# Performance work log

Measured on AMD Instinct MI355X. Metric: run time of the kernel, lower is better.

Reference implementation:

```python
import jax, jax.numpy as jnp
import numpy as np


def conv(x, w, b=None, pad=0):
    y = jax.lax.conv_general_dilated(x, w, (1, 1), [(pad, pad), (pad, pad)],
                                     dimension_numbers=('NCHW', 'OIHW', 'NCHW'))
    if b is not None:
        y = y + b[None, :, None, None]
    return y


def bn(x, g, b, m, v, eps=1e-5):
    scale = g / jnp.sqrt(v + eps)
    return (x - m[None, :, None, None]) * scale[None, :, None, None] + b[None, :, None, None]


def channel_gate(x, w1, b1, w2, b2):
    # avg pool -> MLP -> sigmoid, returns [B, C, 1, 1]
    p = x.mean(axis=(2, 3))                       # [B, C]
    h = jax.nn.relu(p @ w1.T + b1)                # [B, C//r]
    a = h @ w2.T + b2                             # [B, C]
    return jax.nn.sigmoid(a)[:, :, None, None]


def setup_inputs() -> dict:
    key = jax.random.key(0)
    ks = iter(jax.random.split(key, 48))
    B, Cin, H, W = 2, 256, 64, 64
    Ci = Cin // 2          # inter_channels = 128
    Cr = Ci // 16          # gate bottleneck = 8
    def nrm(shape, s=0.05):
        return jax.random.normal(next(ks), shape, jnp.float32) * s
    d = {}
    d['q'] = jax.random.normal(next(ks), (B, Cin, H, W), jnp.float32)
    d['s'] = jax.random.normal(next(ks), (B, Cin, H, W), jnp.float32)
    # Trans_s: conv3x3 + BN
    d['ts_w'] = nrm((Ci, Cin, 3, 3)); d['ts_b'] = jnp.zeros(Ci)
    d['ts_g'] = jnp.ones(Ci); d['ts_be'] = jnp.zeros(Ci)
    d['ts_m'] = nrm((Ci,), 0.01); d['ts_v'] = jnp.ones(Ci)
    # Trans_q: conv3x3 + BN
    d['tq_w'] = nrm((Ci, Cin, 3, 3)); d['tq_b'] = jnp.zeros(Ci)
    d['tq_g'] = jnp.ones(Ci); d['tq_be'] = jnp.zeros(Ci)
    d['tq_m'] = nrm((Ci,), 0.01); d['tq_v'] = jnp.ones(Ci)
    # common_v 1x1
    d['cv_w'] = nrm((Ci, Ci, 1, 1)); d['cv_b'] = jnp.zeros(Ci)
    # key/query 1x1 projections (out = Ci//2)
    d['k1_w'] = nrm((Ci // 2, Ci, 1, 1)); d['k1_b'] = jnp.zeros(Ci // 2)
    d['q1_w'] = nrm((Ci // 2, Ci, 1, 1)); d['q1_b'] = jnp.zeros(Ci // 2)
    d['k2_w'] = nrm((Ci // 2, Ci, 1, 1)); d['k2_b'] = jnp.zeros(Ci // 2)
    d['q2_w'] = nrm((Ci // 2, Ci, 1, 1)); d['q2_b'] = jnp.zeros(Ci // 2)
    # ChannelGate MLP
    d['g1_w'] = nrm((Cr, Ci)); d['g1_b'] = jnp.zeros(Cr)
    d['g2_w'] = nrm((Ci, Cr)); d['g2_b'] = jnp.zeros(Ci)
    # conv_cat: conv3x3 (no bias) + BN
    d['cc_w'] = nrm((Ci, 2 * Ci, 3, 3))
    d['cc_g'] = jnp.ones(Ci); d['cc_be'] = jnp.zeros(Ci)
    d['cc_m'] = nrm((Ci,), 0.01); d['cc_v'] = jnp.ones(Ci)
    return d


def reference(q, s, ts_w, ts_b, ts_g, ts_be, ts_m, ts_v,
              tq_w, tq_b, tq_g, tq_be, tq_m, tq_v,
              cv_w, cv_b, k1_w, k1_b, q1_w, q1_b, k2_w, k2_b, q2_w, q2_b,
              g1_w, g1_b, g2_w, g2_b, cc_w, cc_g, cc_be, cc_m, cc_v):
    # stems: conv3x3 + BN + ReLU
    s = jax.nn.relu(bn(conv(s, ts_w, ts_b, pad=1), ts_g, ts_be, ts_m, ts_v))
    q = jax.nn.relu(bn(conv(q, tq_w, tq_b, pad=1), tq_g, tq_be, tq_m, tq_v))
    B, C, H, W = q.shape
    N = H * W
    # values
    v_q1 = conv(q, cv_w, cv_b)                          # [B,C,H,W]
    v_s1 = conv(s, cv_w, cv_b)
    v_q = v_q1.reshape(B, C, N).transpose(0, 2, 1)      # [B,N,C]
    v_s = v_s1.reshape(B, C, N).transpose(0, 2, 1)
    # dual keys / queries with negation trick
    k1 = conv(s, k1_w, k1_b).reshape(B, C // 2, N)
    k2 = conv(q, k2_w, k2_b).reshape(B, C // 2, N)
    key_cat = jnp.concatenate([k1, -k2], axis=1).transpose(0, 2, 1)   # [B,N,C]
    q1x = conv(s, q1_w, q1_b).reshape(B, C // 2, N)
    q2x = conv(q, q2_w, q2_b).reshape(B, C // 2, N)
    query_cat = jnp.concatenate([q1x, q2x], axis=1)                    # [B,C,N]
    # abs-score attention, dual softmax from the same score matrix
    A_s = jnp.abs(jnp.einsum('bnc,bcm->bnm', key_cat, query_cat))      # [B,N,N]
    att_s = jax.nn.softmax(A_s, axis=-1)
    att_q = jax.nn.softmax(A_s.transpose(0, 2, 1), axis=-1)
    # attend + channel-gate SE fusion + residual
    p_s = jnp.einsum('bnm,bmc->bnc', att_s, v_s).transpose(0, 2, 1).reshape(B, C, H, W)
    E_s = channel_gate(v_s1, g1_w, g1_b, g2_w, g2_b) * p_s + s
    q_s = jnp.einsum('bnm,bmc->bnc', att_q, v_q).transpose(0, 2, 1).reshape(B, C, H, W)
    E_q = channel_gate(v_q1, g1_w, g1_b, g2_w, g2_b) * q_s + q
    # concat + conv3x3(no bias) + BN + ReLU
    cpam = jax.nn.relu(bn(conv(jnp.concatenate([E_q, E_s], axis=1), cc_w, None, pad=1),
                          cc_g, cc_be, cc_m, cc_v))
    return (cpam, E_q, E_s)
```

## Files before the change

### kernel.cpp

```cpp
#include <hip/hip_runtime.h>

typedef __bf16 bf16;
typedef __bf16 v8bf __attribute__((ext_vector_type(8)));
typedef __bf16 v4bf __attribute__((ext_vector_type(4)));
typedef float v4f __attribute__((ext_vector_type(4)));

#define MFMA16(a, b, c) __builtin_amdgcn_mfma_f32_16x16x32_bf16(a, b, c, 0, 0, 0)

__device__ __forceinline__ float sf(float x) {
  if (!(x == x)) return 0.f;
  return fminf(fmaxf(x, -1e30f), 1e30f);
}

__global__ __launch_bounds__(256) void fill_kernel(float* __restrict__ out, float v, int n) {
  int i = blockIdx.x * 256 + threadIdx.x;
  if (i < n) out[i] = v;
}

__global__ __launch_bounds__(256) void prep_kernel(
    const float* __restrict__ ts_w, const float* __restrict__ tq_w,
    const float* ts_b, const float* ts_g, const float* ts_be, const float* ts_m, const float* ts_v,
    const float* tq_b, const float* tq_g, const float* tq_be, const float* tq_m, const float* tq_v,
    bf16* __restrict__ Wt01, float* __restrict__ ss01)
{
  int idx = blockIdx.x * 256 + threadIdx.x;
  if (idx < 589824) {
    int which = idx / 294912;
    int rem = idx - which * 294912;
    int co = rem / 2304;
    int r2 = rem - co * 2304;
    int tap = r2 >> 8;
    int ci = r2 & 255;
    const float* W = which ? tq_w : ts_w;
    Wt01[idx] = (bf16)W[(co * 256 + ci) * 9 + tap];
  } else if (idx < 590080) {
    int i = idx - 589824;
    int which = i >> 7, c = i & 127;
    float g, be, m, vv, bias;
    if (which == 0) { g=ts_g[c]; be=ts_be[c]; m=ts_m[c]; vv=ts_v[c]; bias=ts_b[c]; }
    else            { g=tq_g[c]; be=tq_be[c]; m=tq_m[c]; vv=tq_v[c]; bias=tq_b[c]; }
    float scale = g / sqrtf(vv + 1e-5f);
    ss01[which * 256 + c] = sf(scale);
    ss01[which * 256 + 128 + c] = sf((bias - m) * scale + be);
  }
}

__global__ __launch_bounds__(256) void prep2_kernel(
    const float* __restrict__ cc_w, const float* cc_g, const float* cc_be,
    const float* cc_m, const float* cc_v,
    bf16* __restrict__ Wt2, float* __restrict__ ss_cc)
{
  int idx = blockIdx.x * 256 + threadIdx.x;
  if (idx < 294912) {
    int co = idx / 2304;
    int r2 = idx - co * 2304;
    int tap = r2 >> 8;
    int ci = r2 & 255;
    Wt2[idx] = (bf16)cc_w[(co * 256 + ci) * 9 + tap];
  } else if (idx < 295040) {
    int c = idx - 294912;
    float scale = cc_g[c] / sqrtf(cc_v[c] + 1e-5f);
    ss_cc[c] = sf(scale);
    ss_cc[128 + c] = sf(-cc_m[c] * scale + cc_be[c]);
  }
}

__global__ __launch_bounds__(256) void convN_kernel(
    const float* __restrict__ pS, const float* __restrict__ pQ,
    const bf16* __restrict__ Wb, const float* __restrict__ ssb,
    void* __restrict__ out_, int mode)
{
  __shared__ bf16 As[66][40];
  __shared__ bf16 Bs[3][64][40];

  int y = blockIdx.x;
  int co0 = blockIdx.y * 64;
  int z = blockIdx.z;
  int tsr = z >> 1, b = z & 1;

  const float *in0, *in1;
  const bf16* W;
  const float* sp;
  if (mode == 0) {
    const float* base = (tsr ? pQ : pS) + (long)b * 1048576;
    in0 = base; in1 = base + 524288;
    W = Wb + (long)tsr * 294912;
    sp = ssb + tsr * 256;
  } else {
    in0 = pS + 1048576 + (long)b * 524288;
    in1 = pS + 2097152 + (long)b * 524288;
    W = Wb; sp = ssb;
  }

  int t = threadIdx.x, lane = t & 63, w = t >> 6;
  int l15 = lane & 15, l4 = lane >> 4;
  int wr = (w & 1) * 32, wc = (w >> 1) * 32;
  int ac = t & 31, ag = t >> 5;
  int bco = t >> 2, bk = (t & 3) * 8;

  v4f acc[2][2] = {};

  auto loadA = [&](int it, v8bf& areg) {
    int dy = it >> 3, ks = it & 7;
    int ysrc = y + dy - 1;
    int cg = ks * 32 + ac;
    const float* ip = (cg < 128) ? (in0 + (long)cg * 4096) : (in1 + (long)(cg - 128) * 4096);
    if ((unsigned)ysrc < 64u) {
      const float* src = ip + ysrc * 64 + ag * 8;
#pragma unroll
      for (int i = 0; i < 8; ++i) areg[i] = (bf16)src[i];
    } else {
#pragma unroll
      for (int i = 0; i < 8; ++i) areg[i] = (bf16)0.f;
    }
  };
  auto loadB = [&](int it, v8bf* breg) {
    int dy = it >> 3, ks = it & 7;
    const bf16* wk = W + (long)(co0 + bco) * 2304 + dy * 3 * 256 + ks * 32 + bk;
#pragma unroll
    for (int d = 0; d < 3; ++d) breg[d] = *(const v8bf*)(wk + d * 256);
  };

  v8bf areg, breg[3];
  loadA(0, areg);
  loadB(0, breg);

  for (int it = 0; it < 24; ++it) {
    __syncthreads();
#pragma unroll
    for (int i = 0; i < 8; ++i) As[ag * 8 + 1 + i][ac] = areg[i];
    if (ag == 0) As[0][ac] = (bf16)0.f;
    if (ag == 7) As[65][ac] = (bf16)0.f;
#pragma unroll
    for (int d = 0; d < 3; ++d) *(v8bf*)&Bs[d][bco][bk] = breg[d];
    __syncthreads();
    if (it < 23) { loadA(it + 1, areg); loadB(it + 1, breg); }
#pragma unroll
    for (int d = 0; d < 3; ++d) {
      v8bf af0 = *(const v8bf*)&As[wr + d + l15][l4 * 8];
      v8bf af1 = *(const v8bf*)&As[wr + 16 + d + l15][l4 * 8];
#pragma unroll
      for (int j = 0; j < 2; ++j) {
        v8bf bfr = *(const v8bf*)&Bs[d][wc + j * 16 + l15][l4 * 8];
        acc[0][j] = MFMA16(af0, bfr, acc[0][j]);
        acc[1][j] = MFMA16(af1, bfr, acc[1][j]);
      }
    }
  }
#pragma unroll
  for (int i = 0; i < 2; ++i) {
    int nb = y * 64 + wr + i * 16 + l4 * 4;
#pragma unroll
    for (int j = 0; j < 2; ++j) {
      int c = co0 + wc + j * 16 + l15;
      float scale = sp[c], shift = sp[128 + c];
      if (mode == 0) {
        bf16* o = (bf16*)out_ + ((long)(tsr * 2 + b) * 4096 + nb) * 128 + c;
#pragma unroll
        for (int r = 0; r < 4; ++r)
          o[r * 128] = (bf16)sf(fmaxf(acc[i][j][r] * scale + shift, 0.f));
      } else {
        v4f pk;
#pragma unroll
        for (int r = 0; r < 4; ++r)
          pk[r] = sf(fmaxf(acc[i][j][r] * scale + shift, 0.f));
        *(v4f*)((float*)out_ + ((long)b * 128 + c) * 4096 + nb) = pk;
      }
    }
  }
}

__global__ __launch_bounds__(256) void conv1_kernel(
    const bf16* __restrict__ feat_base,
    const float* __restrict__ cv_w, const float* __restrict__ k1_w, const float* __restrict__ q1_w,
    const float* __restrict__ k2_w, const float* __restrict__ q2_w,
    const float* __restrict__ cv_b, const float* __restrict__ k1_b, const float* __restrict__ q1_b,
    const float* __restrict__ k2_b, const float* __restrict__ q2_b,
    bf16* __restrict__ v_base, bf16* __restrict__ keyT, bf16* __restrict__ queryT,
    float* __restrict__ pmean)
{
  int nt = blockIdx.x;
  int br = blockIdx.z >> 1, b = blockIdx.z & 1;
  long zid = br * 2 + b;
  const bf16* feat = feat_base + zid * 524288 + (long)nt * 4096;

  __shared__ bf16 As[32][40];
  __shared__ bf16 Bs[256][40];

  int t = threadIdx.x, lane = t & 63, w = t >> 6;
  int l15 = lane & 15, l4 = lane >> 4;
  int wr = (w & 1) * 16, wc = (w >> 1) * 128;

  const float* wrow;
  bool negk = false;
  if (t < 128)       wrow = cv_w + (long)t * 128;
  else if (t < 192) { wrow = (br ? k2_w : k1_w) + (long)(t - 128) * 128; negk = (br != 0); }
  else               wrow = (br ? q2_w : q1_w) + (long)(t - 192) * 128;

  v4f acc[8] = {};
  int ap = t >> 2, ak = (t & 3) * 8;

  for (int ks = 0; ks < 4; ++ks) {
    int ci0 = ks * 32;
    v8bf av;
    if (t < 128) av = *(const v8bf*)(feat + ap * 128 + ci0 + ak);
    float wv[32];
#pragma unroll
    for (int u = 0; u < 32; ++u) wv[u] = wrow[ci0 + u];
    if (negk) {
#pragma unroll
      for (int u = 0; u < 32; ++u) wv[u] = -wv[u];
    }
    __syncthreads();
    if (t < 128) *(v8bf*)&As[ap][ak] = av;
#pragma unroll
    for (int u = 0; u < 32; ++u) Bs[t][u] = (bf16)wv[u];
    __syncthreads();
    v8bf af = *(const v8bf*)&As[wr + l15][l4 * 8];
#pragma unroll
    for (int j = 0; j < 8; ++j) {
      v8bf bfr = *(const v8bf*)&Bs[wc + j * 16 + l15][l4 * 8];
      acc[j] = MFMA16(af, bfr, acc[j]);
    }
  }

  int nb = nt * 32 + wr + l4 * 4;
#pragma unroll
  for (int j = 0; j < 8; ++j) {
    int c = wc + j * 16 + l15;
    float bv;
    if (c < 128)      bv = cv_b[c];
    else if (c < 192) bv = br ? -k2_b[c - 128] : k1_b[c - 128];
    else              bv = (br ? q2_b : q1_b)[c - 192];
    float v0 = sf(acc[j][0] + bv), v1 = sf(acc[j][1] + bv);
    float v2 = sf(acc[j][2] + bv), v3 = sf(acc[j][3] + bv);
    if (c < 128) {
      long off = (long)(nb >> 5) * 4096 + (c >> 4) * 512 + ((nb >> 3) & 3) * 128 +
                 (c & 15) * 8 + (nb & 7);
      v4bf pk;
      pk[0] = (bf16)v0; pk[1] = (bf16)v1; pk[2] = (bf16)v2; pk[3] = (bf16)v3;
      *(v4bf*)(v_base + zid * 524288 + off) = pk;
      float s = v0 + v1 + v2 + v3;
      s += __shfl_xor(s, 16, 64);
      s += __shfl_xor(s, 32, 64);
      if (l4 == 0) atomicAdd(&pmean[zid * 128 + c], s);
    } else if (c < 192) {
      int cc = (c - 128) + br * 64;
      long off = (long)(nb >> 4) * 2048 + (cc >> 5) * 512 + ((cc >> 3) & 3) * 128 +
                 (nb & 15) * 8 + (cc & 7);
      bf16* kp = keyT + (long)b * 524288 + off;
      kp[0] = (bf16)v0; kp[8] = (bf16)v1; kp[16] = (bf16)v2; kp[24] = (bf16)v3;
    } else {
      int cc = (c - 192) + br * 64;
      long off = (long)(nb >> 4) * 2048 + (cc >> 5) * 512 + ((cc >> 3) & 3) * 128 +
                 (nb & 15) * 8 + (cc & 7);
      bf16* qp = queryT + (long)b * 524288 + off;
      qp[0] = (bf16)v0; qp[8] = (bf16)v1; qp[16] = (bf16)v2; qp[24] = (bf16)v3;
    }
  }
}

__global__ __launch_bounds__(128) void gate2_kernel(
    const float* __restrict__ pmean, const float* __restrict__ g1_w, const float* __restrict__ g1_b,
    const float* __restrict__ g2_w, const float* __restrict__ g2_b, float* __restrict__ gate)
{
  __shared__ float p[128];
  __shared__ float h[8];
  int z = blockIdx.x, t = threadIdx.x;
  p[t] = pmean[z * 128 + t] * (1.f / 4096.f);
  __syncthreads();
  if (t < 8) {
    float a = g1_b[t];
    for (int c = 0; c < 128; ++c) a += g1_w[t * 128 + c] * p[c];
    h[t] = fmaxf(a, 0.f);
  }
  __syncthreads();
  float a = g2_b[t];
#pragma unroll
  for (int j = 0; j < 8; ++j) a += g2_w[t * 8 + j] * h[j];
  gate[z * 128 + t] = sf(1.f / (1.f + __expf(-a)));
}

__global__ __launch_bounds__(256, 2) void apply_kernel(
    const bf16* __restrict__ keyT, const bf16* __restrict__ queryT,
    const bf16* __restrict__ v_base, const float* __restrict__ gate,
    const bf16* __restrict__ feat_base, float* __restrict__ d_out)
{
  int nt = blockIdx.x, br = blockIdx.z >> 1, b = blockIdx.z & 1;
  int n0 = nt * 32;
  const bf16* Xf = (br ? queryT : keyT) + (long)b * 524288 + (long)(n0 >> 4) * 2048;
  const bf16* Yf = (br ? keyT : queryT) + (long)b * 524288;
  const bf16* Vf = v_base + (long)(br * 2 + b) * 524288;
  const float* gt = gate + (br * 2 + b) * 128;
  const bf16* feat = feat_base + (long)(br * 2 + b) * 524288 + (long)n0 * 128;

  __shared__ bf16 Ps[2][32][72];
  __shared__ float rps[4][32];

  int t = threadIdx.x, lane = t & 63, w = t >> 6;
  int l15 = lane & 15, l4 = lane >> 4;
  int wm = w * 16;
  int wr = (w & 1) * 16;
  int wc = (w >> 1) * 64;

  v8bf af[2][4];
#pragma unroll
  for (int i = 0; i < 2; ++i)
#pragma unroll
    for (int k = 0; k < 4; ++k)
      af[i][k] = *(const v8bf*)(Xf + i * 2048 + k * 512 + lane * 8);

  v4f acc[4] = {};
  float rp[2][4] = {};

  auto loadBy = [&](int m0, v8bf* by) {
    const bf16* p = Yf + (long)((m0 >> 4) + w) * 2048 + lane * 8;
#pragma unroll
    for (int k = 0; k < 4; ++k) by[k] = *(const v8bf*)(p + k * 512);
  };
  auto loadVb = [&](int m0, v8bf* vb) {
    const bf16* p = Vf + (long)(m0 >> 5) * 4096 + ((w >> 1) * 4) * 512 + lane * 8;
#pragma unroll
    for (int j = 0; j < 4; ++j)
#pragma unroll
      for (int k = 0; k < 2; ++k)
        vb[j * 2 + k] = *(const v8bf*)(p + k * 4096 + j * 512);
  };

  v8bf byA[4], byB[4], vbA[8], vbB[8];
  loadBy(0, byA);
  loadVb(0, vbA);

  auto subiter = [&](v8bf (&by)[4], v8bf (&vb)[8], v8bf (&byN)[4], v8bf (&vbN)[8],
                     int psb, int m0n, bool pf) {
    v4f sacc[2] = {};
#pragma unroll
    for (int k = 0; k < 4; ++k)
#pragma unroll
      for (int i = 0; i < 2; ++i)
        sacc[i] = MFMA16(af[i][k], by[k], sacc[i]);
    if (pf) { loadBy(m0n, byN); loadVb(m0n, vbN); }
#pragma unroll
    for (int i = 0; i < 2; ++i)
#pragma unroll
      for (int r = 0; r < 4; ++r) {
        float e = __expf(fminf(fabsf(sacc[i][r]), 80.f) - 50.f);
        rp[i][r] += e;
        Ps[psb][i * 16 + l4 * 4 + r][wm + l15] = (bf16)e;
      }
    asm volatile("s_waitcnt lgkmcnt(0)" ::: "memory");
    __builtin_amdgcn_s_barrier();
#pragma unroll
    for (int k = 0; k < 2; ++k) {
      v8bf p0 = *(const v8bf*)&Ps[psb][wr + l15][k * 32 + l4 * 8];
#pragma unroll
      for (int j = 0; j < 4; ++j)
        acc[j] = MFMA16(p0, vb[j * 2 + k], acc[j]);
    }
  };

  for (int mt2 = 0; mt2 < 32; ++mt2) {
    int mA = mt2 * 128;
    subiter(byA, vbA, byB, vbB, 0, mA + 64, true);
    subiter(byB, vbB, byA, vbA, 1, mA + 128, mt2 < 31);
  }

#pragma unroll
  for (int i = 0; i < 2; ++i)
#pragma unroll
    for (int r = 0; r < 4; ++r) {
      float v = rp[i][r];
      v += __shfl_xor(v, 1, 64);
      v += __shfl_xor(v, 2, 64);
      v += __shfl_xor(v, 4, 64);
      v += __shfl_xor(v, 8, 64);
      if (l15 == 0) rps[w][i * 16 + l4 * 4 + r] = v;
    }
  __syncthreads();

  float* outE = d_out + (long)(br ? 1 : 2) * 1048576 + (long)b * 524288;
  int rowt = wr + l4 * 4;
  float dv[4];
#pragma unroll
  for (int r = 0; r < 4; ++r)
    dv[r] = fmaxf(rps[0][rowt + r] + rps[1][rowt + r] + rps[2][rowt + r] + rps[3][rowt + r],
                  1e-30f);
#pragma unroll
  for (int j = 0; j < 4; ++j) {
    int c = wc + j * 16 + l15;
    float g = gt[c];
    v4f pk;
#pragma unroll
    for (int r = 0; r < 4; ++r) {
      float val = acc[j][r] / dv[r] * g + (float)feat[(long)(rowt + r) * 128 + c];
      pk[r] = sf(val);
    }
    *(v4f*)(outE + (long)c * 4096 + n0 + rowt) = pk;
  }
}

extern "C" void kernel_launch(void* const* d_in, const int* in_sizes, int n_in,
                              void* d_out, int out_size, void* d_ws, size_t ws_size,
                              hipStream_t stream)
{
  if (n_in != 33 || in_sizes[0] != 2097152 || in_sizes[2] != 294912 ||
      in_sizes[14] != 16384 || out_size != 3145728) {
    fill_kernel<<<12288, 256, 0, stream>>>((float*)d_out, 100.0f, 3145728);
    return;
  }
  if (ws_size < 12582912) {
    fill_kernel<<<12288, 256, 0, stream>>>((float*)d_out, 1.0f, 3145728);
    return;
  }

  const float* q_in = (const float*)d_in[0];
  const float* s_in = (const float*)d_in[1];
  char* ob = (char*)d_out;
  float* outf = (float*)d_out;

  float* gate  = (float*)(ob + 0);
  float* pmean = (float*)(ob + 2048);

  char* ws = (char*)d_ws;
  bf16*  sfeat  = (bf16*)(ws + 0);
  bf16*  vs     = (bf16*)(ws + 4194304);
  bf16*  keyT   = (bf16*)(ws + 8388608);
  bf16*  queryT = (bf16*)(ws + 10485760);
  bf16*  Wt01   = (bf16*)(ws + 8388608);
  float* ss01   = (float*)(ws + 10485760);
  bf16*  Wt2    = (bf16*)(ws + 0);
  float* ss_cc  = (float*)(ws + 589824);

  prep_kernel<<<2306, 256, 0, stream>>>(
      (const float*)d_in[2], (const float*)d_in[8],
      (const float*)d_in[3], (const float*)d_in[4], (const float*)d_in[5],
      (const float*)d_in[6], (const float*)d_in[7],
      (const float*)d_in[9], (const float*)d_in[10], (const float*)d_in[11],
      (const float*)d_in[12], (const float*)d_in[13],
      Wt01, ss01);

  fill_kernel<<<2, 256, 0, stream>>>(pmean, 0.0f, 512);

  convN_kernel<<<dim3(64, 2, 4), 256, 0, stream>>>(s_in, q_in, Wt01, ss01, sfeat, 0);

  conv1_kernel<<<dim3(128, 1, 4), 256, 0, stream>>>(
      sfeat,
      (const float*)d_in[14], (const float*)d_in[16], (const float*)d_in[18],
      (const float*)d_in[20], (const float*)d_in[22],
      (const float*)d_in[15], (const float*)d_in[17], (const float*)d_in[19],
      (const float*)d_in[21], (const float*)d_in[23],
      vs, keyT, queryT, pmean);

  gate2_kernel<<<4, 128, 0, stream>>>(pmean, (const float*)d_in[24], (const float*)d_in[25],
                                      (const float*)d_in[26], (const float*)d_in[27], gate);

  apply_kernel<<<dim3(128, 1, 4), 256, 0, stream>>>(keyT, queryT, vs, gate, sfeat, outf);

  prep2_kernel<<<1153, 256, 0, stream>>>(
      (const float*)d_in[28], (const float*)d_in[29], (const float*)d_in[30],
      (const float*)d_in[31], (const float*)d_in[32], Wt2, ss_cc);

  convN_kernel<<<dim3(64, 2, 2), 256, 0, stream>>>(outf, nullptr, Wt2, ss_cc, outf, 1);
}
```

Baseline: 275.3 us.

## Pre-transpose conv inputs to channel-last bf16 for vectorized A loads

Adds a transpose kernel that converts the s and q inputs from NCHW fp32 into a channel-last bf16 buffer placed in the output region. The 3x3 conv kernel then loads its A tile as single 16-byte vectors instead of eight strided fp32 loads with conversion, and writes shared memory with one vector store. The apply kernel now also writes its fused E outputs back into the bf16 feature buffer in channel-last layout, so the final conv reads bf16 from workspace rather than fp32 NCHW from the output. This costs an extra transpose pass and extra bf16 writes, and it relocates the Wt2 and ss_cc scratch buffers.

```diff
diff --git a/kernel.cpp b/kernel.cpp
--- a/kernel.cpp
+++ b/kernel.cpp
@@ -65,8 +65,27 @@
   }
 }
 
+__global__ __launch_bounds__(256) void tr_kernel(
+    const float* __restrict__ s_in, const float* __restrict__ q_in, bf16* __restrict__ xin)
+{
+  int nb = blockIdx.x;
+  int z = blockIdx.y;
+  const float* in = ((z >> 1) ? q_in : s_in) + (long)(z & 1) * 1048576;
+  bf16* out = xin + (long)z * 1048576;
+  int t = threadIdx.x, lane = t & 63, w = t >> 6;
+  long n = (long)nb * 64 + lane;
+#pragma unroll
+  for (int i = 0; i < 8; ++i) {
+    int c8 = w * 8 + i;
+    v8bf o;
+#pragma unroll
+    for (int j = 0; j < 8; ++j) o[j] = (bf16)in[(long)(c8 * 8 + j) * 4096 + n];
+    *(v8bf*)(out + n * 256 + c8 * 8) = o;
+  }
+}
+
 __global__ __launch_bounds__(256) void convN_kernel(
-    const float* __restrict__ pS, const float* __restrict__ pQ,
+    const bf16* __restrict__ inA,
     const bf16* __restrict__ Wb, const float* __restrict__ ssb,
     void* __restrict__ out_, int mode)
 {
@@ -78,24 +97,24 @@
   int z = blockIdx.z;
   int tsr = z >> 1, b = z & 1;
 
-  const float *in0, *in1;
+  const bf16 *in0, *in1;
   const bf16* W;
   const float* sp;
   if (mode == 0) {
-    const float* base = (tsr ? pQ : pS) + (long)b * 1048576;
-    in0 = base; in1 = base + 524288;
+    in0 = inA + (long)z * 1048576;
+    in1 = nullptr;
     W = Wb + (long)tsr * 294912;
     sp = ssb + tsr * 256;
   } else {
-    in0 = pS + 1048576 + (long)b * 524288;
-    in1 = pS + 2097152 + (long)b * 524288;
+    in0 = inA + (long)(2 + b) * 524288;
+    in1 = inA + (long)b * 524288;
     W = Wb; sp = ssb;
   }
 
   int t = threadIdx.x, lane = t & 63, w = t >> 6;
   int l15 = lane & 15, l4 = lane >> 4;
   int wr = (w & 1) * 32, wc = (w >> 1) * 32;
-  int ac = t & 31, ag = t >> 5;
+  int ax = t >> 2, ac0 = (t & 3) * 8;
   int bco = t >> 2, bk = (t & 3) * 8;
 
   v4f acc[2][2] = {};
@@ -103,12 +122,14 @@
   auto loadA = [&](int it, v8bf& areg) {
     int dy = it >> 3, ks = it & 7;
     int ysrc = y + dy - 1;
-    int cg = ks * 32 + ac;
-    const float* ip = (cg < 128) ? (in0 + (long)cg * 4096) : (in1 + (long)(cg - 128) * 4096);
     if ((unsigned)ysrc < 64u) {
-      const float* src = ip + ysrc * 64 + ag * 8;
-#pragma unroll
-      for (int i = 0; i < 8; ++i) areg[i] = (bf16)src[i];
+      long n = (long)ysrc * 64 + ax;
+      int cg = ks * 32 + ac0;
+      const bf16* src;
+      if (mode == 0)     src = in0 + n * 256 + cg;
+      else if (cg < 128) src = in0 + n * 128 + cg;
+      else               src = in1 + n * 128 + (cg - 128);
+      areg = *(const v8bf*)src;
     } else {
 #pragma unroll
       for (int i = 0; i < 8; ++i) areg[i] = (bf16)0.f;
@@ -121,16 +142,16 @@
     for (int d = 0; d < 3; ++d) breg[d] = *(const v8bf*)(wk + d * 256);
   };
 
+  if (t < 32) As[0][t] = (bf16)0.f;
+  else if (t < 64) As[65][t - 32] = (bf16)0.f;
+
   v8bf areg, breg[3];
   loadA(0, areg);
   loadB(0, breg);
 
   for (int it = 0; it < 24; ++it) {
     __syncthreads();
-#pragma unroll
-    for (int i = 0; i < 8; ++i) As[ag * 8 + 1 + i][ac] = areg[i];
-    if (ag == 0) As[0][ac] = (bf16)0.f;
-    if (ag == 7) As[65][ac] = (bf16)0.f;
+    *(v8bf*)&As[ax + 1][ac0] = areg;
 #pragma unroll
     for (int d = 0; d < 3; ++d) *(v8bf*)&Bs[d][bco][bk] = breg[d];
     __syncthreads();
@@ -284,7 +305,7 @@
 __global__ __launch_bounds__(256, 2) void apply_kernel(
     const bf16* __restrict__ keyT, const bf16* __restrict__ queryT,
     const bf16* __restrict__ v_base, const float* __restrict__ gate,
-    const bf16* __restrict__ feat_base, float* __restrict__ d_out)
+    bf16* __restrict__ feat_base, float* __restrict__ d_out)
 {
   int nt = blockIdx.x, br = blockIdx.z >> 1, b = blockIdx.z & 1;
   int n0 = nt * 32;
@@ -292,7 +313,7 @@
   const bf16* Yf = (br ? keyT : queryT) + (long)b * 524288;
   const bf16* Vf = v_base + (long)(br * 2 + b) * 524288;
   const float* gt = gate + (br * 2 + b) * 128;
-  const bf16* feat = feat_base + (long)(br * 2 + b) * 524288 + (long)n0 * 128;
+  bf16* feat = feat_base + (long)(br * 2 + b) * 524288 + (long)n0 * 128;
 
   __shared__ bf16 Ps[2][32][72];
   __shared__ float rps[4][32];
@@ -392,8 +413,11 @@
     v4f pk;
 #pragma unroll
     for (int r = 0; r < 4; ++r) {
-      float val = acc[j][r] / dv[r] * g + (float)feat[(long)(rowt + r) * 128 + c];
-      pk[r] = sf(val);
+      long fi = (long)(rowt + r) * 128 + c;
+      float fv = (float)feat[fi];
+      float val = sf(acc[j][r] / dv[r] * g + fv);
+      pk[r] = val;
+      feat[fi] = (bf16)val;
     }
     *(v4f*)(outE + (long)c * 4096 + n0 + rowt) = pk;
   }
@@ -420,6 +444,7 @@
 
   float* gate  = (float*)(ob + 0);
   float* pmean = (float*)(ob + 2048);
+  bf16*  xin   = (bf16*)(ob + 4194304);
 
   char* ws = (char*)d_ws;
   bf16*  sfeat  = (bf16*)(ws + 0);
@@ -428,8 +453,8 @@
   bf16*  queryT = (bf16*)(ws + 10485760);
   bf16*  Wt01   = (bf16*)(ws + 8388608);
   float* ss01   = (float*)(ws + 10485760);
-  bf16*  Wt2    = (bf16*)(ws + 0);
-  float* ss_cc  = (float*)(ws + 589824);
+  bf16*  Wt2    = (bf16*)(ws + 8388608);
+  float* ss_cc  = (float*)(ws + 8978432);
 
   prep_kernel<<<2306, 256, 0, stream>>>(
       (const float*)d_in[2], (const float*)d_in[8],
@@ -441,7 +466,9 @@
 
   fill_kernel<<<2, 256, 0, stream>>>(pmean, 0.0f, 512);
 
-  convN_kernel<<<dim3(64, 2, 4), 256, 0, stream>>>(s_in, q_in, Wt01, ss01, sfeat, 0);
+  tr_kernel<<<dim3(64, 4), 256, 0, stream>>>(s_in, q_in, xin);
+
+  convN_kernel<<<dim3(64, 2, 4), 256, 0, stream>>>(xin, Wt01, ss01, sfeat, 0);
 
   conv1_kernel<<<dim3(128, 1, 4), 256, 0, stream>>>(
       sfeat,
@@ -460,5 +487,5 @@
       (const float*)d_in[28], (const float*)d_in[29], (const float*)d_in[30],
       (const float*)d_in[31], (const float*)d_in[32], Wt2, ss_cc);
 
-  convN_kernel<<<dim3(64, 2, 2), 256, 0, stream>>>(outf, nullptr, Wt2, ss_cc, outf, 1);
-}
+  convN_kernel<<<dim3(64, 2, 2), 256, 0, stream>>>(sfeat, Wt2, ss_cc, outf, 1);
+}
```

New measurement: 266.1 us. 3.3% less time.
